# Kernel optimization log

Measured on AMD Instinct MI355X. Metric: run time of the kernel, lower is better.

## Reference

```python
import jax, jax.numpy as jnp
import numpy as np

GAMMA = 1.0
T = 2.0
EPS = 1e-8

def setup_inputs() -> dict:
    key = jax.random.key(0)
    k1, k2 = jax.random.split(key)
    N, D = 8192, 64
    user_vecs = jax.random.normal(k1, (N, D), dtype=jnp.float32)
    item_vecs = jax.random.normal(k2, (N, D), dtype=jnp.float32)
    return {"user_vecs": user_vecs, "item_vecs": item_vecs}

def _normalize(x):
    return x / jnp.linalg.norm(x, axis=-1, keepdims=True)

def _alignment(u, i):
    u = _normalize(u)
    i = _normalize(i)
    return jnp.mean(jnp.sum((u - i) ** 2, axis=1))

def _uniformity(x):
    # log( mean_{i<j} exp(-t * ||x_i - x_j||^2) + eps ) with normalized x.
    # For unit vectors ||x_i - x_j||^2 = 2 - 2 <x_i, x_j>. Use full symmetric
    # Gram matrix: sum over off-diagonal = 2 * sum over i<j; diag contributes
    # exp(0) = 1 per row, so subtract N, divide by N*(N-1).
    x = _normalize(x)
    n = x.shape[0]
    gram = x @ x.T                       # [N, N]
    sq_pdist = jnp.maximum(2.0 - 2.0 * gram, 0.0)
    total = jnp.sum(jnp.exp(-T * sq_pdist))
    mean_pair = (total - n) / (n * (n - 1))
    return jnp.log(mean_pair + EPS)

def reference(user_vecs, item_vecs):
    align = _alignment(user_vecs, item_vecs)
    uniform = GAMMA * (_uniformity(user_vecs) + _uniformity(item_vecs)) / 2.0
    return align + uniform
```

## Files before the change

### kernel.cpp

```cpp
#include <hip/hip_runtime.h>
#include <cstdint>


#define NROWS 8192
#define DIM 64
#define NT2 32
#define GRAM_SLOTS (NT2 * (NT2 + 1))
#define K1_BLOCKS 512

static constexpr float EXP_SCALE = 5.770780163555852f;
static constexpr float EPS_F = 1e-8f;

typedef __bf16 bf16x8 __attribute__((ext_vector_type(8)));
typedef float f32x4 __attribute__((ext_vector_type(4)));

__device__ __forceinline__ unsigned short f32_to_bf16_rn(float f) {
    union { float f; uint32_t u; } c; c.f = f;
    uint32_t u = c.u;
    uint32_t r = u + 0x7FFFu + ((u >> 16) & 1u);
    return (unsigned short)(r >> 16);
}

__global__ void __launch_bounds__(256) normalize_align_kernel(
    const float* __restrict__ user, const float* __restrict__ item,
    unsigned short* __restrict__ xu, unsigned short* __restrict__ xi,
    float* __restrict__ pa)
{
    const int wave = threadIdx.x >> 6;
    const int lane = threadIdx.x & 63;
    const int wid  = blockIdx.x * 4 + wave;

    float asum = 0.0f;
    #pragma unroll
    for (int r = 0; r < 4; ++r) {
        const int idx = (wid * 4 + r) * DIM + lane;
        float u = user[idx];
        float v = item[idx];
        float su = u * u, sv = v * v;
        #pragma unroll
        for (int m = 1; m < 64; m <<= 1) {
            su += __shfl_xor(su, m, 64);
            sv += __shfl_xor(sv, m, 64);
        }
        float iu = rsqrtf(su); iu = iu * (1.5f - 0.5f * su * iu * iu);
        float iv = rsqrtf(sv); iv = iv * (1.5f - 0.5f * sv * iv * iv);
        float un = u * iu, vn = v * iv;
        xu[idx] = f32_to_bf16_rn(un);
        xi[idx] = f32_to_bf16_rn(vn);
        float d = un - vn;
        asum += d * d;
    }
    #pragma unroll
    for (int m = 1; m < 64; m <<= 1) asum += __shfl_xor(asum, m, 64);
    __shared__ float ws4[4];
    if (lane == 0) ws4[wave] = asum;
    __syncthreads();
    if (threadIdx.x == 0) pa[blockIdx.x] = ws4[0] + ws4[1] + ws4[2] + ws4[3];
}

__global__ void __launch_bounds__(512, 8) gram_exp_kernel(
    const unsigned short* __restrict__ xu,
    const unsigned short* __restrict__ xi,
    float* __restrict__ pg)
{
    const int bx = blockIdx.x, by = blockIdx.y;
    const unsigned short* __restrict__ X;
    int bi, bj;
    if (by < NT2) {
        if (by >= bx) { X = xu; bi = bx; bj = by; }
        else          { X = xi; bi = by; bj = bx; }
    } else            { X = xi; bi = bx; bj = bx; }
    const bool diag = (bi == bj);

    __shared__ unsigned short lds[16384];
    __shared__ float wsum[8];

    const int wave = threadIdx.x >> 6;
    const int lane = threadIdx.x & 63;

    bf16x8 a[2][2];
    {
        const int arow = bi * 256 + wave * 32 + (lane & 15);
        const int acol = (lane >> 4) * 8;
        #pragma unroll
        for (int rb = 0; rb < 2; ++rb)
            #pragma unroll
            for (int ks = 0; ks < 2; ++ks)
                a[rb][ks] = *reinterpret_cast<const bf16x8*>(
                    X + (arow + rb * 16) * DIM + acol + ks * 32);
    }

    {
        const int base = bj * 256;
        #pragma unroll
        for (int i = 0; i < 4; ++i) {
            int n = i * 512 + threadIdx.x;
            int r = n >> 3, c = n & 7;
            bf16x8 v = *reinterpret_cast<const bf16x8*>(X + (base + r) * DIM + c * 8);
            int di = (r >> 4) * 1024 + c * 128 + (r & 15) * 8;
            *reinterpret_cast<bf16x8*>(&lds[di]) = v;
        }
    }
    __syncthreads();

    float l0 = 0.0f, l1 = 0.0f;
    #pragma unroll
    for (int cb = 0; cb < 16; ++cb) {
        bf16x8 b0 = *reinterpret_cast<const bf16x8*>(&lds[cb * 1024 + lane * 8]);
        bf16x8 b1 = *reinterpret_cast<const bf16x8*>(&lds[cb * 1024 + 512 + lane * 8]);
        #pragma unroll
        for (int rb = 0; rb < 2; ++rb) {
            f32x4 c = {0.f, 0.f, 0.f, 0.f};
            c = __builtin_amdgcn_mfma_f32_16x16x32_bf16(a[rb][0], b0, c, 0, 0, 0);
            c = __builtin_amdgcn_mfma_f32_16x16x32_bf16(a[rb][1], b1, c, 0, 0, 0);
            #pragma unroll
            for (int e = 0; e < 4; ++e) {
                float ex = __builtin_amdgcn_exp2f(fmaf(c[e], EXP_SCALE, -EXP_SCALE));
                if (diag) ex = fminf(ex, 1.0f);
                if (e & 1) l1 += ex; else l0 += ex;
            }
        }
    }

    float local = l0 + l1;
    #pragma unroll
    for (int m = 1; m < 64; m <<= 1) local += __shfl_xor(local, m, 64);
    if (lane == 0) wsum[wave] = local;
    __syncthreads();
    if (threadIdx.x == 0) {
        float t = 0.f;
        #pragma unroll
        for (int w = 0; w < 8; ++w) t += wsum[w];
        pg[by * NT2 + bx] = diag ? t : 2.0f * t;
    }
}

__global__ void __launch_bounds__(256) final_kernel(
    const float* __restrict__ pa, const float* __restrict__ pg,
    float* __restrict__ out)
{
    float a = 0.f, su = 0.f, si = 0.f;
    for (int s = threadIdx.x; s < K1_BLOCKS; s += 256) a += pa[s];
    for (int s = threadIdx.x; s < GRAM_SLOTS; s += 256) {
        int bx = s & (NT2 - 1), by = s >> 5;
        bool is_item = (by == NT2) || (by < bx);
        float v = pg[s];
        if (is_item) si += v; else su += v;
    }
    #pragma unroll
    for (int m = 1; m < 64; m <<= 1) {
        a  += __shfl_xor(a,  m, 64);
        su += __shfl_xor(su, m, 64);
        si += __shfl_xor(si, m, 64);
    }
    __shared__ float r[12];
    const int wave = threadIdx.x >> 6, lane = threadIdx.x & 63;
    if (lane == 0) { r[wave] = a; r[4 + wave] = su; r[8 + wave] = si; }
    __syncthreads();
    if (threadIdx.x == 0) {
        float A  = r[0] + r[1] + r[2]  + r[3];
        float SU = r[4] + r[5] + r[6]  + r[7];
        float SI = r[8] + r[9] + r[10] + r[11];
        const float n = (float)NROWS;
        const float denom = n * (n - 1.0f);
        out[0] = A / n + 0.5f * (logf((SU - n) / denom + EPS_F)
                               + logf((SI - n) / denom + EPS_F));
    }
}

extern "C" void kernel_launch(void* const* d_in, const int* in_sizes, int n_in,
                              void* d_out, int out_size, void* d_ws, size_t ws_size,
                              hipStream_t stream)
{
    const float* user = (const float*)d_in[0];
    const float* item = (const float*)d_in[1];

    unsigned short* xu = (unsigned short*)d_ws;
    unsigned short* xi = xu + (size_t)NROWS * DIM;
    float* pa = (float*)(xi + (size_t)NROWS * DIM);
    float* pg = pa + K1_BLOCKS;

    normalize_align_kernel<<<K1_BLOCKS, 256, 0, stream>>>(user, item, xu, xi, pa);
    gram_exp_kernel<<<dim3(NT2, NT2 + 1), 512, 0, stream>>>(xu, xi, pg);
    final_kernel<<<1, 256, 0, stream>>>(pa, pg, (float*)d_out);
}
```

Before: 84.64 us.

## Fold exp scale into normalized vectors and fuse final reduction into gram kernel

The exp2 scaling is pre-multiplied into the bf16 normalized vectors as a square-root factor, so each Gram element needs only an exp2 with no FMA. The constant offset becomes a single E4_INV multiply at the end. The separate final kernel is removed: gram blocks atomically accumulate into 16 slots, and the last block, found via an atomic counter, computes the output. The inner loop unroll is reduced to 2. In exchange this adds atomic contention, a non-deterministic summation order, and some bf16 rounding error on the scaled values.

```diff
diff --git a/kernel.cpp b/kernel.cpp
--- a/kernel.cpp
+++ b/kernel.cpp
@@ -8,7 +8,9 @@
 #define GRAM_SLOTS (NT2 * (NT2 + 1))
 #define K1_BLOCKS 512
 
-static constexpr float EXP_SCALE = 5.770780163555852f;
+static constexpr float SQRT_SCALE = 2.4022448309943147f;
+static constexpr float E4        = 54.598150033144236f;
+static constexpr float E4_INV    = 0.018315638888734179f;
 static constexpr float EPS_F = 1e-8f;
 
 typedef __bf16 bf16x8 __attribute__((ext_vector_type(8)));
@@ -24,8 +26,13 @@
 __global__ void __launch_bounds__(256) normalize_align_kernel(
     const float* __restrict__ user, const float* __restrict__ item,
     unsigned short* __restrict__ xu, unsigned short* __restrict__ xi,
-    float* __restrict__ pa)
+    float* __restrict__ pa, float* __restrict__ acc, unsigned* __restrict__ ctr)
 {
+    if (blockIdx.x == 0) {
+        if (threadIdx.x < 16) acc[threadIdx.x] = 0.0f;
+        else if (threadIdx.x == 16) *ctr = 0u;
+    }
+
     const int wave = threadIdx.x >> 6;
     const int lane = threadIdx.x & 63;
     const int wid  = blockIdx.x * 4 + wave;
@@ -45,8 +52,8 @@
         float iu = rsqrtf(su); iu = iu * (1.5f - 0.5f * su * iu * iu);
         float iv = rsqrtf(sv); iv = iv * (1.5f - 0.5f * sv * iv * iv);
         float un = u * iu, vn = v * iv;
-        xu[idx] = f32_to_bf16_rn(un);
-        xi[idx] = f32_to_bf16_rn(vn);
+        xu[idx] = f32_to_bf16_rn(un * SQRT_SCALE);
+        xi[idx] = f32_to_bf16_rn(vn * SQRT_SCALE);
         float d = un - vn;
         asum += d * d;
     }
@@ -61,19 +68,24 @@
 __global__ void __launch_bounds__(512, 8) gram_exp_kernel(
     const unsigned short* __restrict__ xu,
     const unsigned short* __restrict__ xi,
-    float* __restrict__ pg)
+    const float* __restrict__ pa,
+    float* __restrict__ acc, unsigned* __restrict__ ctr,
+    float* __restrict__ out)
 {
     const int bx = blockIdx.x, by = blockIdx.y;
     const unsigned short* __restrict__ X;
     int bi, bj;
+    bool is_item;
     if (by < NT2) {
-        if (by >= bx) { X = xu; bi = bx; bj = by; }
-        else          { X = xi; bi = by; bj = bx; }
-    } else            { X = xi; bi = bx; bj = bx; }
+        if (by >= bx) { X = xu; bi = bx; bj = by; is_item = false; }
+        else          { X = xi; bi = by; bj = bx; is_item = true;  }
+    } else            { X = xi; bi = bx; bj = bx; is_item = true;  }
     const bool diag = (bi == bj);
 
     __shared__ unsigned short lds[16384];
     __shared__ float wsum[8];
+    __shared__ float fin[16];
+    __shared__ bool amLast;
 
     const int wave = threadIdx.x >> 6;
     const int lane = threadIdx.x & 63;
@@ -104,7 +116,7 @@
     __syncthreads();
 
     float l0 = 0.0f, l1 = 0.0f;
-    #pragma unroll
+    #pragma unroll 2
     for (int cb = 0; cb < 16; ++cb) {
         bf16x8 b0 = *reinterpret_cast<const bf16x8*>(&lds[cb * 1024 + lane * 8]);
         bf16x8 b1 = *reinterpret_cast<const bf16x8*>(&lds[cb * 1024 + 512 + lane * 8]);
@@ -115,8 +127,8 @@
             c = __builtin_amdgcn_mfma_f32_16x16x32_bf16(a[rb][1], b1, c, 0, 0, 0);
             #pragma unroll
             for (int e = 0; e < 4; ++e) {
-                float ex = __builtin_amdgcn_exp2f(fmaf(c[e], EXP_SCALE, -EXP_SCALE));
-                if (diag) ex = fminf(ex, 1.0f);
+                float ex = __builtin_amdgcn_exp2f(c[e]);
+                if (diag) ex = fminf(ex, E4);
                 if (e & 1) l1 += ex; else l0 += ex;
             }
         }
@@ -131,40 +143,36 @@
         float t = 0.f;
         #pragma unroll
         for (int w = 0; w < 8; ++w) t += wsum[w];
-        pg[by * NT2 + bx] = diag ? t : 2.0f * t;
+        t = diag ? t : 2.0f * t;
+        atomicAdd(&acc[(is_item ? 8 : 0) + (bx & 7)], t);
+        __threadfence();
+        unsigned prev = atomicAdd(ctr, 1u);
+        amLast = (prev == GRAM_SLOTS - 1);
     }
-}
+    __syncthreads();
 
-__global__ void __launch_bounds__(256) final_kernel(
-    const float* __restrict__ pa, const float* __restrict__ pg,
-    float* __restrict__ out)
-{
-    float a = 0.f, su = 0.f, si = 0.f;
-    for (int s = threadIdx.x; s < K1_BLOCKS; s += 256) a += pa[s];
-    for (int s = threadIdx.x; s < GRAM_SLOTS; s += 256) {
-        int bx = s & (NT2 - 1), by = s >> 5;
-        bool is_item = (by == NT2) || (by < bx);
-        float v = pg[s];
-        if (is_item) si += v; else su += v;
-    }
-    #pragma unroll
-    for (int m = 1; m < 64; m <<= 1) {
-        a  += __shfl_xor(a,  m, 64);
-        su += __shfl_xor(su, m, 64);
-        si += __shfl_xor(si, m, 64);
-    }
-    __shared__ float r[12];
-    const int wave = threadIdx.x >> 6, lane = threadIdx.x & 63;
-    if (lane == 0) { r[wave] = a; r[4 + wave] = su; r[8 + wave] = si; }
-    __syncthreads();
-    if (threadIdx.x == 0) {
-        float A  = r[0] + r[1] + r[2]  + r[3];
-        float SU = r[4] + r[5] + r[6]  + r[7];
-        float SI = r[8] + r[9] + r[10] + r[11];
-        const float n = (float)NROWS;
-        const float denom = n * (n - 1.0f);
-        out[0] = A / n + 0.5f * (logf((SU - n) / denom + EPS_F)
-                               + logf((SI - n) / denom + EPS_F));
+    if (amLast) {
+        __threadfence();
+        float av = pa[threadIdx.x];
+        #pragma unroll
+        for (int m = 1; m < 64; m <<= 1) av += __shfl_xor(av, m, 64);
+        if (lane == 0) wsum[wave] = av;
+        if (threadIdx.x < 16)
+            fin[threadIdx.x] = atomicAdd(&acc[threadIdx.x], 0.0f);
+        __syncthreads();
+        if (threadIdx.x == 0) {
+            float A = 0.f;
+            #pragma unroll
+            for (int w = 0; w < 8; ++w) A += wsum[w];
+            float su = 0.f, si = 0.f;
+            #pragma unroll
+            for (int s = 0; s < 8; ++s) { su += fin[s]; si += fin[8 + s]; }
+            su *= E4_INV; si *= E4_INV;
+            const float n = (float)NROWS;
+            const float denom = n * (n - 1.0f);
+            out[0] = A / n + 0.5f * (logf((su - n) / denom + EPS_F)
+                                   + logf((si - n) / denom + EPS_F));
+        }
     }
 }
 
@@ -177,10 +185,12 @@
 
     unsigned short* xu = (unsigned short*)d_ws;
     unsigned short* xi = xu + (size_t)NROWS * DIM;
-    float* pa = (float*)(xi + (size_t)NROWS * DIM);
-    float* pg = pa + K1_BLOCKS;
+    float* pa  = (float*)(xi + (size_t)NROWS * DIM);
+    float* acc = pa + K1_BLOCKS;
+    unsigned* ctr = (unsigned*)(acc + 16);
 
-    normalize_align_kernel<<<K1_BLOCKS, 256, 0, stream>>>(user, item, xu, xi, pa);
-    gram_exp_kernel<<<dim3(NT2, NT2 + 1), 512, 0, stream>>>(xu, xi, pg);
-    final_kernel<<<1, 256, 0, stream>>>(pa, pg, (float*)d_out);
+    normalize_align_kernel<<<K1_BLOCKS, 256, 0, stream>>>(user, item, xu, xi,
+                                                          pa, acc, ctr);
+    gram_exp_kernel<<<dim3(NT2, NT2 + 1), 512, 0, stream>>>(xu, xi, pa, acc,
+                                                            ctr, (float*)d_out);
 }
```

Result: slower. 88.37 us (+4.4%).
